# Optimization experiments

Hardware: AMD Instinct MI355X
Metric: run time of the kernel (lower is better)

The kernel has to match this reference:

```python
import jax, jax.numpy as jnp
import numpy as np

NEIGHBOUR_NUM = 8  # args.neighbour_num


def _sqrdis_map(x, y):
    # x: [B,M,3], y: [B,N,3] -> [B,M,N] squared distances
    x2 = jnp.sum(x * x, axis=-1)
    y2 = jnp.sum(y * y, axis=-1)
    inner = jnp.einsum('bmd,bnd->bmn', x, y)
    return x2[:, :, None] + y2[:, None, :] - 2.0 * inner


def _chamfer(x, y):
    d = _sqrdis_map(x, y)
    return d.min(axis=2), d.min(axis=1)


def _neighbor_index(v, k):
    # torch.topk(dist, k+1, largest=False) then drop self
    d = _sqrdis_map(v, v)
    idx = jax.lax.top_k(-d, k + 1)[1]  # ascending distance order
    return idx[:, :, 1:]


def _arap(idx, dp, sp):
    B = dp.shape[0]
    bid = jnp.arange(B)[:, None, None]
    dn = dp[bid, idx] - dp[:, :, None, :]  # [B,N,K,3]
    sn = sp[bid, idx] - sp[:, :, None, :]
    dd = jnp.sqrt(jnp.sum(dn * dn, axis=-1) + 1e-5)
    sd = jnp.sqrt(jnp.sum(sn * sn, axis=-1) + 1e-5)
    diff = dd - sd
    return jnp.sum(diff * diff) / B


def setup_inputs() -> dict:
    key = jax.random.key(0)
    ks = jax.random.split(key, 7)
    T, B, N = 3, 4, 4096
    return {
        'phi': jax.random.normal(ks[0], (T, B, 1024), dtype=jnp.float32),
        'point_weight': jax.random.normal(ks[1], (T, B, N, 1), dtype=jnp.float32),
        'deform_rigid_points': 0.5 * jax.random.normal(ks[2], (T, B, N, 3), dtype=jnp.float32),
        'deformation_points': 0.5 * jax.random.normal(ks[3], (T, B, N, 3), dtype=jnp.float32),
        'rigid_matrix': 0.1 * jax.random.normal(ks[4], (T, B, 4, 4), dtype=jnp.float32),
        'source_points': jax.random.uniform(ks[5], (B, N, 3), dtype=jnp.float32, minval=-1.0, maxval=1.0),
        'target_points': jax.random.uniform(ks[6], (B, N, 3), dtype=jnp.float32, minval=-1.0, maxval=1.0),
    }


def reference(phi, point_weight, deform_rigid_points, deformation_points,
              rigid_matrix, source_points, target_points):
    B = source_points.shape[0]
    T = phi.shape[0]  # iter_time = len(phi_list)
    idx = _neighbor_index(source_points, NEIGHBOUR_NUM)
    trans_mask = jnp.zeros((4, 4), dtype=rigid_matrix.dtype).at[0:3, 3].set(1.0)
    total = jnp.asarray(0.0, dtype=source_points.dtype)
    for t in range(T):  # small fixed iter count, structurally distinct stages
        dp = deformation_points[t]
        # loss_on_cd
        d1, d2 = _chamfer(dp, target_points)
        cd = (jnp.sum(d1) + jnp.sum(d2)) * 0.5 / B
        # loss_on_pd (rigid-deformed vs full deformation)
        diff = deform_rigid_points[t] - dp
        pd = jnp.sum(diff * diff) / B
        # loss_on_sparse
        sp = jnp.mean(jnp.abs(point_weight[t]))
        # loss_on_tran
        tr = trans_mask[None] * rigid_matrix[t]
        tran = jnp.sum(tr * tr) / B
        # loss_on_arap
        ar = _arap(idx, dp, source_points)
        total = total + cd + pd + sp + tran + ar
    return total
```

## Files before the change

### kernel.cpp

```cpp
#include <hip/hip_runtime.h>

#define T_ 3
#define B_ 4
#define N_ 4096
#define K_ 8

template <int NW>
__device__ inline float block_reduce(float v, float* scratch) {
    #pragma unroll
    for (int off = 32; off > 0; off >>= 1) v += __shfl_down(v, off, 64);
    const int lane = threadIdx.x & 63, wid = threadIdx.x >> 6;
    if (lane == 0) scratch[wid] = v;
    __syncthreads();
    float s = 0.f;
    if (threadIdx.x == 0) {
        #pragma unroll
        for (int w = 0; w < NW; ++w) s += scratch[w];
    }
    return s;
}

__device__ inline unsigned f2sortable(float f) {
    unsigned b = __float_as_uint(f);
    return b ^ ((unsigned)((int)b >> 31) | 0x80000000u);
}
__device__ inline float sortable2f(unsigned u) {
    unsigned b = (u & 0x80000000u) ? (u ^ 0x80000000u) : ~u;
    return __uint_as_float(b);
}

#define CE_(A, i, j) { unsigned lo_ = min(A[i], A[j]); A[j] = max(A[i], A[j]); A[i] = lo_; }
__device__ inline void sort8(unsigned s[8]) {
    CE_(s,0,1) CE_(s,2,3) CE_(s,4,5) CE_(s,6,7)
    CE_(s,0,2) CE_(s,1,3) CE_(s,4,6) CE_(s,5,7)
    CE_(s,1,2) CE_(s,5,6)
    CE_(s,0,4) CE_(s,1,5) CE_(s,2,6) CE_(s,3,7)
    CE_(s,2,4) CE_(s,3,5)
    CE_(s,1,2) CE_(s,3,4) CE_(s,5,6)
}
__device__ inline void merge_top8(unsigned a[8], const unsigned s[8]) {
    #pragma unroll
    for (int i = 0; i < 8; ++i) a[i] = min(a[i], s[7 - i]);
    CE_(a,0,4) CE_(a,1,5) CE_(a,2,6) CE_(a,3,7)
    CE_(a,0,2) CE_(a,1,3) CE_(a,4,6) CE_(a,5,7)
    CE_(a,0,1) CE_(a,2,3) CE_(a,4,5) CE_(a,6,7)
}

#define KQPB 8
#define KWIN 1024

__global__ __launch_bounds__(256, 8) void knn_kernel(const float* __restrict__ src,
                                                     int* __restrict__ idx,
                                                     unsigned* __restrict__ cmin,
                                                     float* __restrict__ out) {
    __shared__ float4 win[KWIN];
    const int g = blockIdx.x * 256 + threadIdx.x;
    if (g < T_ * B_ * 2 * N_) cmin[g] = 0xFFFFFFFFu;
    if (g == 0) *out = 0.f;

    const int b  = blockIdx.x / (N_ / KQPB);
    const int q0 = (blockIdx.x % (N_ / KQPB)) * KQPB;
    const float* sb = src + (size_t)b * N_ * 3;

    const int lq = threadIdx.x >> 5;
    const int c  = threadIdx.x & 31;
    const int i  = q0 + lq;
    const float qx = sb[3 * i], qy = sb[3 * i + 1], qz = sb[3 * i + 2];
    const float q2 = fmaf(qx, qx, fmaf(qy, qy, qz * qz));

    unsigned a[K_];
    #pragma unroll
    for (int p = 0; p < K_; ++p) a[p] = 0xFFFFFFFFu;

    for (int w = 0; w < N_ / KWIN; ++w) {
        __syncthreads();
        for (int j = threadIdx.x; j < KWIN; j += 256) {
            int jg = w * KWIN + j;
            float x = sb[3 * jg], y = sb[3 * jg + 1], z = sb[3 * jg + 2];
            win[j] = make_float4(-2.f * x, -2.f * y, -2.f * z, fmaf(x, x, fmaf(y, y, z * z)));
        }
        __syncthreads();

        #pragma unroll
        for (int bt = 0; bt < KWIN / 8 / 32; ++bt) {
            unsigned s[8];
            #pragma unroll
            for (int u = 0; u < 8; ++u) {
                int jl = 32 * (bt * 8 + u) + c;
                float4 cd = win[jl];
                float d = fmaf(qx, cd.x, fmaf(qy, cd.y, fmaf(qz, cd.z, cd.w))) + q2;
                int jglob = w * KWIN + jl;
                unsigned pu = (__float_as_uint(d) & 0xFFFFF000u) | (unsigned)jglob;
                s[u] = (jglob == i) ? 0xFFFFFFFFu : pu;
            }
            sort8(s);
            merge_top8(a, s);
        }
    }
    __syncthreads();

    unsigned* sm = (unsigned*)win;
    for (int half = 16; half >= 1; half >>= 1) {
        #pragma unroll
        for (int e = 0; e < K_; ++e) sm[288 * e + 9 * c + lq] = a[e];
        __syncthreads();
        if (c < half) {
            unsigned s[8];
            #pragma unroll
            for (int e = 0; e < K_; ++e) s[e] = sm[288 * e + 9 * (c + half) + lq];
            merge_top8(a, s);
        }
        __syncthreads();
    }

    if (c == 0) {
        int* op = idx + ((size_t)b * N_ + q0 + lq) * K_;
        #pragma unroll
        for (int k = 0; k < K_; ++k) op[k] = (int)(a[k] & 0xFFFu);
    }
}

#define CCH 32
#define CCHSZ (N_ / CCH)
#define CQ 4

__global__ __launch_bounds__(256, 8) void chamfer_kernel(const float* __restrict__ dp_all,
                                                         const float* __restrict__ tp,
                                                         unsigned* __restrict__ cmin) {
    __shared__ float4 pts[CCHSZ];
    int blk = blockIdx.x;
    const int cc = blk & (CCH - 1); blk >>= 5;
    const int qc = blk & 3;         blk >>= 2;
    const int tbd = blk;
    const int dir = tbd & 1;
    const int tb  = tbd >> 1;
    const int b = tb % B_, t = tb / B_;

    const float* dpb = dp_all + ((size_t)(t * B_ + b)) * N_ * 3;
    const float* tpb = tp + (size_t)b * N_ * 3;
    const float* dbase = dir ? dpb : tpb;
    const float* qbase = dir ? tpb : dpb;

    if (threadIdx.x < CCHSZ) {
        int jg = cc * CCHSZ + threadIdx.x;
        float x = dbase[3 * jg], y = dbase[3 * jg + 1], z = dbase[3 * jg + 2];
        pts[threadIdx.x] = make_float4(-2.f * x, -2.f * y, -2.f * z,
                                       fmaf(x, x, fmaf(y, y, z * z)));
    }
    __syncthreads();

    float qx[CQ], qy[CQ], qz[CQ], m[CQ];
    #pragma unroll
    for (int u = 0; u < CQ; ++u) {
        int q = qc * 1024 + u * 256 + threadIdx.x;
        qx[u] = qbase[3 * q]; qy[u] = qbase[3 * q + 1]; qz[u] = qbase[3 * q + 2];
        m[u] = 3.4e38f;
    }
    #pragma unroll 4
    for (int j = 0; j < CCHSZ; ++j) {
        float4 cd = pts[j];
        #pragma unroll
        for (int u = 0; u < CQ; ++u)
            m[u] = fminf(m[u], fmaf(qx[u], cd.x, fmaf(qy[u], cd.y, fmaf(qz[u], cd.z, cd.w))));
    }
    unsigned* cm = cmin + (size_t)tbd * N_ + qc * 1024;
    #pragma unroll
    for (int u = 0; u < CQ; ++u)
        atomicMin(&cm[u * 256 + threadIdx.x], f2sortable(m[u]));
}

__global__ __launch_bounds__(256) void finalize_kernel(const float* __restrict__ dp_all,
                                                       const float* __restrict__ tp,
                                                       const float* __restrict__ src,
                                                       const int* __restrict__ idx,
                                                       const unsigned* __restrict__ cmin,
                                                       const float* __restrict__ drp,
                                                       const float* __restrict__ pw,
                                                       const float* __restrict__ rm,
                                                       float* __restrict__ out) {
    __shared__ float red[4];
    const int blk = blockIdx.x;

    if (blk < 384) {
        const int tbd = blk >> 4;
        const int q = (blk & 15) * 256 + threadIdx.x;
        const int dir = tbd & 1, tb = tbd >> 1, b = tb % B_, t = tb / B_;
        const float* qbase = dir ? tp + (size_t)b * N_ * 3
                                 : dp_all + ((size_t)(t * B_ + b)) * N_ * 3;
        float mrel = sortable2f(cmin[(size_t)tbd * N_ + q]);
        float x = qbase[3 * q], y = qbase[3 * q + 1], z = qbase[3 * q + 2];
        float v = fmaf(x, x, fmaf(y, y, z * z)) + mrel;
        float s = block_reduce<4>(v, red);
        if (threadIdx.x == 0) atomicAdd(out, s * (0.5f / B_));
    } else if (blk < 576) {
        const int ab = blk - 384;
        const int chunk = ab & 15;
        const int tb = ab >> 4;
        const int b = tb % B_, t = tb / B_;
        const int n = chunk * 256 + threadIdx.x;
        const float* dp = dp_all + ((size_t)t * B_ + b) * (N_ * 3);
        const float* sp = src + (size_t)b * (N_ * 3);
        const float px = dp[n * 3], py = dp[n * 3 + 1], pz = dp[n * 3 + 2];
        const float sx = sp[n * 3], sy = sp[n * 3 + 1], sz = sp[n * 3 + 2];
        const int* ip = idx + ((size_t)b * N_ + n) * K_;
        float acc = 0.f;
        #pragma unroll
        for (int k = 0; k < K_; ++k) {
            int j = ip[k];
            float dx = dp[j * 3] - px, dy = dp[j * 3 + 1] - py, dz = dp[j * 3 + 2] - pz;
            float ex = sp[j * 3] - sx, ey = sp[j * 3 + 1] - sy, ez = sp[j * 3 + 2] - sz;
            float dd = sqrtf(fmaf(dx, dx, fmaf(dy, dy, dz * dz)) + 1e-5f);
            float sd = sqrtf(fmaf(ex, ex, fmaf(ey, ey, ez * ez)) + 1e-5f);
            float df = dd - sd;
            acc = fmaf(df, df, acc);
        }
        float s = block_reduce<4>(acc, red);
        if (threadIdx.x == 0) atomicAdd(out, s * (1.0f / B_));
    } else {
        const int PD_N = T_ * B_ * N_ * 3;
        const int SP_N = T_ * B_ * N_;
        const int stride = 32 * 256;
        const int gid = (blk - 576) * 256 + threadIdx.x;
        float apd = 0.f;
        for (int i = gid; i < PD_N; i += stride) {
            float d = drp[i] - dp_all[i];
            apd = fmaf(d, d, apd);
        }
        float asp = 0.f;
        for (int i = gid; i < SP_N; i += stride) asp += fabsf(pw[i]);
        float atr = 0.f;
        if (gid < T_ * B_ * 3) {
            int t = gid / (B_ * 3);
            int b = (gid / 3) % B_;
            int r = gid % 3;
            float v = rm[t * B_ * 16 + b * 16 + r * 4 + 3];
            atr = v * v;
        }
        float acc = apd * (1.0f / B_) + asp * (1.0f / (B_ * N_)) + atr * (1.0f / B_);
        float s = block_reduce<4>(acc, red);
        if (threadIdx.x == 0) atomicAdd(out, s);
    }
}

extern "C" void kernel_launch(void* const* d_in, const int* in_sizes, int n_in,
                              void* d_out, int out_size, void* d_ws, size_t ws_size,
                              hipStream_t stream) {
    const float* pw  = (const float*)d_in[1];
    const float* drp = (const float*)d_in[2];
    const float* dp  = (const float*)d_in[3];
    const float* rm  = (const float*)d_in[4];
    const float* sp  = (const float*)d_in[5];
    const float* tp  = (const float*)d_in[6];
    float* out = (float*)d_out;

    int*      idx  = (int*)d_ws;
    unsigned* cmin = (unsigned*)((char*)d_ws + (size_t)B_ * N_ * K_ * 4);

    knn_kernel<<<B_ * (N_ / KQPB), 256, 0, stream>>>(sp, idx, cmin, out);
    chamfer_kernel<<<T_ * B_ * 2 * 4 * CCH, 256, 0, stream>>>(dp, tp, cmin);
    finalize_kernel<<<608, 256, 0, stream>>>(dp, tp, sp, idx, cmin, drp, pw, rm, out);
}
```

Baseline: 144.1 us.

## Merge kNN and chamfer into one launch with per-chunk partial minima

Replaces the separate kNN and chamfer kernels with one kernel whose blocks take either role, so the two independent stages can run concurrently and one launch is removed. The kNN part now handles two queries per thread group, 16 queries per block, which reuses each shared-memory candidate load across two queries. The chamfer part doubles the queries per thread. Chamfer results are now written as plain per-chunk partial minima instead of atomicMin on sortable ints, and the finalize kernel reduces the 32 partials per point. This raises workspace traffic and finalize reads, and register pressure rises, with launch bounds lowered to 6 waves.

New measurement: 131.3 us. 1.1x faster.

```diff
diff --git a/kernel.cpp b/kernel.cpp
--- a/kernel.cpp
+++ b/kernel.cpp
@@ -4,6 +4,12 @@
 #define B_ 4
 #define N_ 4096
 #define K_ 8
+
+#define KNN_BLOCKS (B_ * (N_ / 16))
+#define CH_CCH     32
+#define CH_CHSZ    (N_ / CH_CCH)
+#define CH_CQ      8
+#define CH_BLOCKS  (T_ * B_ * 2 * 2 * CH_CCH)
 
 template <int NW>
 __device__ inline float block_reduce(float v, float* scratch) {
@@ -20,15 +26,6 @@
     return s;
 }
 
-__device__ inline unsigned f2sortable(float f) {
-    unsigned b = __float_as_uint(f);
-    return b ^ ((unsigned)((int)b >> 31) | 0x80000000u);
-}
-__device__ inline float sortable2f(unsigned u) {
-    unsigned b = (u & 0x80000000u) ? (u ^ 0x80000000u) : ~u;
-    return __uint_as_float(b);
-}
-
 #define CE_(A, i, j) { unsigned lo_ = min(A[i], A[j]); A[j] = max(A[i], A[j]); A[i] = lo_; }
 __device__ inline void sort8(unsigned s[8]) {
     CE_(s,0,1) CE_(s,2,3) CE_(s,4,5) CE_(s,6,7)
@@ -46,134 +43,145 @@
     CE_(a,0,1) CE_(a,2,3) CE_(a,4,5) CE_(a,6,7)
 }
 
-#define KQPB 8
 #define KWIN 1024
 
-__global__ __launch_bounds__(256, 8) void knn_kernel(const float* __restrict__ src,
-                                                     int* __restrict__ idx,
-                                                     unsigned* __restrict__ cmin,
-                                                     float* __restrict__ out) {
-    __shared__ float4 win[KWIN];
-    const int g = blockIdx.x * 256 + threadIdx.x;
-    if (g < T_ * B_ * 2 * N_) cmin[g] = 0xFFFFFFFFu;
-    if (g == 0) *out = 0.f;
-
-    const int b  = blockIdx.x / (N_ / KQPB);
-    const int q0 = (blockIdx.x % (N_ / KQPB)) * KQPB;
-    const float* sb = src + (size_t)b * N_ * 3;
-
-    const int lq = threadIdx.x >> 5;
-    const int c  = threadIdx.x & 31;
-    const int i  = q0 + lq;
-    const float qx = sb[3 * i], qy = sb[3 * i + 1], qz = sb[3 * i + 2];
-    const float q2 = fmaf(qx, qx, fmaf(qy, qy, qz * qz));
-
-    unsigned a[K_];
-    #pragma unroll
-    for (int p = 0; p < K_; ++p) a[p] = 0xFFFFFFFFu;
-
-    for (int w = 0; w < N_ / KWIN; ++w) {
+__global__ __launch_bounds__(256, 6) void mega_kernel(const float* __restrict__ src,
+                                                      const float* __restrict__ dp_all,
+                                                      const float* __restrict__ tp,
+                                                      int* __restrict__ idx,
+                                                      float* __restrict__ pmin,
+                                                      float* __restrict__ out) {
+    __shared__ unsigned smem_u[4352];
+    if (blockIdx.x == 0 && threadIdx.x == 0) *out = 0.f;
+
+    if (blockIdx.x < KNN_BLOCKS) {
+        float4* win = (float4*)smem_u;
+        const int b  = blockIdx.x / (N_ / 16);
+        const int q0 = (blockIdx.x % (N_ / 16)) * 16;
+        const float* sb = src + (size_t)b * N_ * 3;
+
+        const int qp = threadIdx.x >> 5;
+        const int c  = threadIdx.x & 31;
+        const int i0 = q0 + 2 * qp, i1 = i0 + 1;
+        const float qx0 = sb[3 * i0], qy0 = sb[3 * i0 + 1], qz0 = sb[3 * i0 + 2];
+        const float qx1 = sb[3 * i1], qy1 = sb[3 * i1 + 1], qz1 = sb[3 * i1 + 2];
+        const float q20 = fmaf(qx0, qx0, fmaf(qy0, qy0, qz0 * qz0));
+        const float q21 = fmaf(qx1, qx1, fmaf(qy1, qy1, qz1 * qz1));
+
+        unsigned a0[K_], a1[K_];
+        #pragma unroll
+        for (int p = 0; p < K_; ++p) { a0[p] = 0xFFFFFFFFu; a1[p] = 0xFFFFFFFFu; }
+
+        for (int w = 0; w < N_ / KWIN; ++w) {
+            __syncthreads();
+            for (int j = threadIdx.x; j < KWIN; j += 256) {
+                int jg = w * KWIN + j;
+                float x = sb[3 * jg], y = sb[3 * jg + 1], z = sb[3 * jg + 2];
+                win[j] = make_float4(-2.f * x, -2.f * y, -2.f * z,
+                                     fmaf(x, x, fmaf(y, y, z * z)));
+            }
+            __syncthreads();
+
+            #pragma unroll
+            for (int bt = 0; bt < KWIN / 8 / 32; ++bt) {
+                unsigned s0[8], s1[8];
+                #pragma unroll
+                for (int u = 0; u < 8; ++u) {
+                    int jl = 32 * (bt * 8 + u) + c;
+                    float4 cd = win[jl];
+                    int jglob = w * KWIN + jl;
+                    float d0 = fmaf(qx0, cd.x, fmaf(qy0, cd.y, fmaf(qz0, cd.z, cd.w))) + q20;
+                    float d1 = fmaf(qx1, cd.x, fmaf(qy1, cd.y, fmaf(qz1, cd.z, cd.w))) + q21;
+                    unsigned p0 = (__float_as_uint(d0) & 0xFFFFF000u) | (unsigned)jglob;
+                    unsigned p1 = (__float_as_uint(d1) & 0xFFFFF000u) | (unsigned)jglob;
+                    s0[u] = (jglob == i0) ? 0xFFFFFFFFu : p0;
+                    s1[u] = (jglob == i1) ? 0xFFFFFFFFu : p1;
+                }
+                sort8(s0); merge_top8(a0, s0);
+                sort8(s1); merge_top8(a1, s1);
+            }
+        }
         __syncthreads();
-        for (int j = threadIdx.x; j < KWIN; j += 256) {
-            int jg = w * KWIN + j;
-            float x = sb[3 * jg], y = sb[3 * jg + 1], z = sb[3 * jg + 2];
-            win[j] = make_float4(-2.f * x, -2.f * y, -2.f * z, fmaf(x, x, fmaf(y, y, z * z)));
+
+        unsigned* sm = smem_u;
+        for (int half = 16; half >= 1; half >>= 1) {
+            #pragma unroll
+            for (int e = 0; e < K_; ++e) {
+                sm[(e * 32 + c) * 17 + 2 * qp]     = a0[e];
+                sm[(e * 32 + c) * 17 + 2 * qp + 1] = a1[e];
+            }
+            __syncthreads();
+            if (c < half) {
+                unsigned t0[8], t1[8];
+                #pragma unroll
+                for (int e = 0; e < K_; ++e) {
+                    t0[e] = sm[(e * 32 + c + half) * 17 + 2 * qp];
+                    t1[e] = sm[(e * 32 + c + half) * 17 + 2 * qp + 1];
+                }
+                merge_top8(a0, t0);
+                merge_top8(a1, t1);
+            }
+            __syncthreads();
+        }
+
+        if (c == 0) {
+            int* op0 = idx + ((size_t)b * N_ + i0) * K_;
+            int* op1 = idx + ((size_t)b * N_ + i1) * K_;
+            #pragma unroll
+            for (int k = 0; k < K_; ++k) {
+                op0[k] = (int)(a0[k] & 0xFFFu);
+                op1[k] = (int)(a1[k] & 0xFFFu);
+            }
+        }
+    } else {
+        float4* pts = (float4*)smem_u;
+        int blk = blockIdx.x - KNN_BLOCKS;
+        const int cc = blk & (CH_CCH - 1); blk >>= 5;
+        const int qc = blk & 1;            blk >>= 1;
+        const int tbd = blk;
+        const int dir = tbd & 1;
+        const int tb  = tbd >> 1;
+        const int b = tb % B_, t = tb / B_;
+
+        const float* dpb = dp_all + ((size_t)(t * B_ + b)) * N_ * 3;
+        const float* tpb = tp + (size_t)b * N_ * 3;
+        const float* dbase = dir ? dpb : tpb;
+        const float* qbase = dir ? tpb : dpb;
+
+        if (threadIdx.x < CH_CHSZ) {
+            int jg = cc * CH_CHSZ + threadIdx.x;
+            float x = dbase[3 * jg], y = dbase[3 * jg + 1], z = dbase[3 * jg + 2];
+            pts[threadIdx.x] = make_float4(-2.f * x, -2.f * y, -2.f * z,
+                                           fmaf(x, x, fmaf(y, y, z * z)));
         }
         __syncthreads();
 
-        #pragma unroll
-        for (int bt = 0; bt < KWIN / 8 / 32; ++bt) {
-            unsigned s[8];
-            #pragma unroll
-            for (int u = 0; u < 8; ++u) {
-                int jl = 32 * (bt * 8 + u) + c;
-                float4 cd = win[jl];
-                float d = fmaf(qx, cd.x, fmaf(qy, cd.y, fmaf(qz, cd.z, cd.w))) + q2;
-                int jglob = w * KWIN + jl;
-                unsigned pu = (__float_as_uint(d) & 0xFFFFF000u) | (unsigned)jglob;
-                s[u] = (jglob == i) ? 0xFFFFFFFFu : pu;
-            }
-            sort8(s);
-            merge_top8(a, s);
-        }
+        float qx[CH_CQ], qy[CH_CQ], qz[CH_CQ], m[CH_CQ];
+        #pragma unroll
+        for (int u = 0; u < CH_CQ; ++u) {
+            int q = qc * 2048 + u * 256 + threadIdx.x;
+            qx[u] = qbase[3 * q]; qy[u] = qbase[3 * q + 1]; qz[u] = qbase[3 * q + 2];
+            m[u] = 3.4e38f;
+        }
+        #pragma unroll 2
+        for (int j = 0; j < CH_CHSZ; ++j) {
+            float4 cd = pts[j];
+            #pragma unroll
+            for (int u = 0; u < CH_CQ; ++u)
+                m[u] = fminf(m[u], fmaf(qx[u], cd.x, fmaf(qy[u], cd.y, fmaf(qz[u], cd.z, cd.w))));
+        }
+        float* pm = pmin + ((size_t)tbd * CH_CCH + cc) * N_ + qc * 2048;
+        #pragma unroll
+        for (int u = 0; u < CH_CQ; ++u)
+            pm[u * 256 + threadIdx.x] = m[u];
     }
-    __syncthreads();
-
-    unsigned* sm = (unsigned*)win;
-    for (int half = 16; half >= 1; half >>= 1) {
-        #pragma unroll
-        for (int e = 0; e < K_; ++e) sm[288 * e + 9 * c + lq] = a[e];
-        __syncthreads();
-        if (c < half) {
-            unsigned s[8];
-            #pragma unroll
-            for (int e = 0; e < K_; ++e) s[e] = sm[288 * e + 9 * (c + half) + lq];
-            merge_top8(a, s);
-        }
-        __syncthreads();
-    }
-
-    if (c == 0) {
-        int* op = idx + ((size_t)b * N_ + q0 + lq) * K_;
-        #pragma unroll
-        for (int k = 0; k < K_; ++k) op[k] = (int)(a[k] & 0xFFFu);
-    }
-}
-
-#define CCH 32
-#define CCHSZ (N_ / CCH)
-#define CQ 4
-
-__global__ __launch_bounds__(256, 8) void chamfer_kernel(const float* __restrict__ dp_all,
-                                                         const float* __restrict__ tp,
-                                                         unsigned* __restrict__ cmin) {
-    __shared__ float4 pts[CCHSZ];
-    int blk = blockIdx.x;
-    const int cc = blk & (CCH - 1); blk >>= 5;
-    const int qc = blk & 3;         blk >>= 2;
-    const int tbd = blk;
-    const int dir = tbd & 1;
-    const int tb  = tbd >> 1;
-    const int b = tb % B_, t = tb / B_;
-
-    const float* dpb = dp_all + ((size_t)(t * B_ + b)) * N_ * 3;
-    const float* tpb = tp + (size_t)b * N_ * 3;
-    const float* dbase = dir ? dpb : tpb;
-    const float* qbase = dir ? tpb : dpb;
-
-    if (threadIdx.x < CCHSZ) {
-        int jg = cc * CCHSZ + threadIdx.x;
-        float x = dbase[3 * jg], y = dbase[3 * jg + 1], z = dbase[3 * jg + 2];
-        pts[threadIdx.x] = make_float4(-2.f * x, -2.f * y, -2.f * z,
-                                       fmaf(x, x, fmaf(y, y, z * z)));
-    }
-    __syncthreads();
-
-    float qx[CQ], qy[CQ], qz[CQ], m[CQ];
-    #pragma unroll
-    for (int u = 0; u < CQ; ++u) {
-        int q = qc * 1024 + u * 256 + threadIdx.x;
-        qx[u] = qbase[3 * q]; qy[u] = qbase[3 * q + 1]; qz[u] = qbase[3 * q + 2];
-        m[u] = 3.4e38f;
-    }
-    #pragma unroll 4
-    for (int j = 0; j < CCHSZ; ++j) {
-        float4 cd = pts[j];
-        #pragma unroll
-        for (int u = 0; u < CQ; ++u)
-            m[u] = fminf(m[u], fmaf(qx[u], cd.x, fmaf(qy[u], cd.y, fmaf(qz[u], cd.z, cd.w))));
-    }
-    unsigned* cm = cmin + (size_t)tbd * N_ + qc * 1024;
-    #pragma unroll
-    for (int u = 0; u < CQ; ++u)
-        atomicMin(&cm[u * 256 + threadIdx.x], f2sortable(m[u]));
 }
 
 __global__ __launch_bounds__(256) void finalize_kernel(const float* __restrict__ dp_all,
                                                        const float* __restrict__ tp,
                                                        const float* __restrict__ src,
                                                        const int* __restrict__ idx,
-                                                       const unsigned* __restrict__ cmin,
+                                                       const float* __restrict__ pmin,
                                                        const float* __restrict__ drp,
                                                        const float* __restrict__ pw,
                                                        const float* __restrict__ rm,
@@ -187,7 +195,10 @@
         const int dir = tbd & 1, tb = tbd >> 1, b = tb % B_, t = tb / B_;
         const float* qbase = dir ? tp + (size_t)b * N_ * 3
                                  : dp_all + ((size_t)(t * B_ + b)) * N_ * 3;
-        float mrel = sortable2f(cmin[(size_t)tbd * N_ + q]);
+        float mrel = 3.4e38f;
+        #pragma unroll
+        for (int cc = 0; cc < CH_CCH; ++cc)
+            mrel = fminf(mrel, pmin[((size_t)tbd * CH_CCH + cc) * N_ + q]);
         float x = qbase[3 * q], y = qbase[3 * q + 1], z = qbase[3 * q + 2];
         float v = fmaf(x, x, fmaf(y, y, z * z)) + mrel;
         float s = block_reduce<4>(v, red);
@@ -253,10 +264,9 @@
     const float* tp  = (const float*)d_in[6];
     float* out = (float*)d_out;
 
-    int*      idx  = (int*)d_ws;
-    unsigned* cmin = (unsigned*)((char*)d_ws + (size_t)B_ * N_ * K_ * 4);
-
-    knn_kernel<<<B_ * (N_ / KQPB), 256, 0, stream>>>(sp, idx, cmin, out);
-    chamfer_kernel<<<T_ * B_ * 2 * 4 * CCH, 256, 0, stream>>>(dp, tp, cmin);
-    finalize_kernel<<<608, 256, 0, stream>>>(dp, tp, sp, idx, cmin, drp, pw, rm, out);
-}
+    int*   idx  = (int*)d_ws;
+    float* pmin = (float*)((char*)d_ws + (size_t)B_ * N_ * K_ * 4);
+
+    mega_kernel<<<KNN_BLOCKS + CH_BLOCKS, 256, 0, stream>>>(sp, dp, tp, idx, pmin, out);
+    finalize_kernel<<<608, 256, 0, stream>>>(dp, tp, sp, idx, pmin, drp, pw, rm, out);
+}
```
